# Kernel optimization log

Measured on AMD Instinct MI355X. Metric: run time of the kernel, lower is better.

The kernel has to match this reference:

```python
import jax, jax.numpy as jnp
import numpy as np

N_WAY = 64

def setup_inputs() -> dict:
    key = jax.random.key(0)
    k1, k2, k3, k4 = jax.random.split(key, 4)
    S, Q, F, D = 1024, 16384, 2048, 512
    xs = jax.random.normal(k1, (S, F), dtype=jnp.float32)
    ys = jax.random.randint(k2, (S,), 0, N_WAY, dtype=jnp.int64)
    xq = jax.random.normal(k3, (Q, F), dtype=jnp.float32)
    W = jax.random.normal(k4, (F, D), dtype=jnp.float32) * 0.02
    b = jnp.zeros((D,), dtype=jnp.float32)
    return {"xs": xs, "ys": ys, "xq": xq, "W": W, "b": b}

def reference(xs, ys, xq, W, b):
    # encoder: linear projection [*, F] -> [*, D]
    z_s = xs @ W + b            # [S, D]
    z_q = xq @ W + b            # [Q, D]
    # class prototypes: segment mean over support embeddings -> [N_way, D]
    counts = jax.ops.segment_sum(jnp.ones_like(ys, dtype=z_s.dtype), ys, num_segments=N_WAY)
    proto = jax.ops.segment_sum(z_s, ys, num_segments=N_WAY) / jnp.clip(counts, 1.0)[:, None]
    # pairwise squared euclidean distance (expand + pow + sum), [Q, N_way]
    diff = z_q[:, None, :] - proto[None, :, :]   # [Q, N_way, D]
    dists = jnp.sum(diff * diff, axis=-1)
    return -dists
```

## Files before the change

### kernel.cpp

```cpp
#include <hip/hip_runtime.h>


typedef __attribute__((ext_vector_type(8))) short short8;
typedef __attribute__((ext_vector_type(4))) float floatx4;

#define S_ROWS 1024
#define F_DIM  2048
#define D_DIM  512
#define NWAY   64
#define Q_ROWS 16384

static __device__ __forceinline__ unsigned short f2bf(float f) {
  unsigned int u = __float_as_uint(f);
  u += 0x7FFF + ((u >> 16) & 1);
  return (unsigned short)(u >> 16);
}
static __device__ __forceinline__ float bf2f(unsigned short s) {
  return __uint_as_float(((unsigned int)s) << 16);
}
static __device__ __forceinline__ unsigned int pack_bf2(float x, float y) {
  unsigned int ux = __float_as_uint(x) + 0x8000u;
  unsigned int uy = __float_as_uint(y) + 0x8000u;
  return __builtin_amdgcn_perm(uy, ux, 0x07060302u);
}

static __device__ __forceinline__ void load_lds16(const unsigned short* g, unsigned short* l) {
  __builtin_amdgcn_global_load_lds((const __attribute__((address_space(1))) unsigned int*)g,
                                   (__attribute__((address_space(3))) unsigned int*)l,
                                   16, 0, 0);
}

__global__ __launch_bounds__(256) void k_prep(const float* __restrict__ W,
                                              unsigned short* __restrict__ Wt,
                                              float* __restrict__ outz,
                                              float* __restrict__ proto_acc,
                                              const int* __restrict__ ys,
                                              int* __restrict__ order,
                                              int* __restrict__ starts,
                                              float* __restrict__ counts) {
  __shared__ unsigned short t[64][65];
  __shared__ int cnt[NWAY];
  __shared__ int st[NWAY + 1];
  __shared__ int wp[NWAY];
  int bx = blockIdx.x;
  int tid = threadIdx.x;
  if (bx < 256) {
    int f0 = (bx >> 3) << 6;
    int d0 = (bx & 7) << 6;
    for (int j = 0; j < 16; j++) {
      int lin = j * 256 + tid;
      int fl = lin >> 6, dl = lin & 63;
      t[fl][dl] = f2bf(W[(size_t)(f0 + fl) * 512 + d0 + dl]);
    }
    __syncthreads();
    for (int j = 0; j < 16; j++) {
      int lin = j * 256 + tid;
      int dl = lin >> 6, fl = lin & 63;
      Wt[(size_t)(d0 + dl) * 2048 + f0 + fl] = t[fl][dl];
    }
    float4 zz = {0.f, 0.f, 0.f, 0.f};
#pragma unroll
    for (int p = 0; p < 4; p++)
      *(float4*)&outz[(size_t)bx * 4096 + p * 1024 + tid * 4] = zz;
    if (tid < 128) proto_acc[bx * 128 + tid] = 0.f;
  } else {
    if (tid < NWAY) cnt[tid] = 0;
    __syncthreads();
    for (int j = tid; j < S_ROWS; j += 256) atomicAdd(&cnt[ys[j]], 1);
    __syncthreads();
    if (tid == 0) {
      int a = 0;
      for (int c = 0; c < NWAY; c++) { st[c] = a; wp[c] = a; a += cnt[c]; }
      st[NWAY] = a;
    }
    __syncthreads();
    for (int j = tid; j < S_ROWS; j += 256) {
      int c = ys[j];
      int p = atomicAdd(&wp[c], 1);
      order[p] = j;
    }
    if (tid < NWAY) counts[tid] = (float)cnt[tid];
    if (tid < NWAY + 1) starts[tid] = st[tid];
  }
}

__global__ __launch_bounds__(256) void k1_csum(const float* __restrict__ xs,
                                               const int* __restrict__ order,
                                               const int* __restrict__ starts,
                                               float* __restrict__ csum) {
  __shared__ int lord[S_ROWS];
  int c = blockIdx.x >> 1;
  int tid = threadIdx.x;
  int s = starts[c], e = starts[c + 1];
  int len = e - s;
  for (int j = tid; j < len; j += 256) lord[j] = order[s + j];
  __syncthreads();
  int f0 = (blockIdx.x & 1) * 1024 + tid * 4;
  float4 a = {0.f, 0.f, 0.f, 0.f};
  for (int i = 0; i < len; i++) {
    float4 v = *(const float4*)&xs[(size_t)lord[i] * F_DIM + f0];
    a.x += v.x; a.y += v.y; a.z += v.z; a.w += v.w;
  }
  *(float4*)&csum[(size_t)c * F_DIM + f0] = a;
}

__global__ __launch_bounds__(256) void k2_proto(const float* __restrict__ W,
                                               const float* __restrict__ csum,
                                               float* __restrict__ proto_acc) {
  __shared__ float cs[256];
  int bx = blockIdx.x;
  int c = bx >> 4;
  int dh = ((bx >> 3) & 1) * 256;
  int fc = (bx & 7) * 256;
  int tid = threadIdx.x;
  cs[tid] = csum[(size_t)c * F_DIM + fc + tid];
  __syncthreads();
  float a0 = 0.f;
#pragma unroll 8
  for (int f = 0; f < 256; f++)
    a0 += cs[f] * W[(size_t)(fc + f) * 512 + dh + tid];
  atomicAdd(&proto_acc[c * 512 + dh + tid], a0);
}

__global__ __launch_bounds__(256) void k2b_finalize(const float* __restrict__ proto_acc,
                                                    const float* __restrict__ b,
                                                    const float* __restrict__ counts,
                                                    unsigned short* __restrict__ proto_bf,
                                                    float* __restrict__ pnorm_part) {
  __shared__ float red[256];
  int n = blockIdx.x, tid = threadIdx.x;
  float cntv = counts[n];
  float inv = 1.f / fmaxf(cntv, 1.f);
  float qsq[2];
#pragma unroll
  for (int h = 0; h < 2; h++) {
    int d = h * 256 + tid;
    float p = (proto_acc[n * 512 + d] + cntv * b[d]) * inv;
    unsigned short hh = f2bf(p);
    proto_bf[(size_t)n * 512 + d] = hh;
    float q = bf2f(hh);
    qsq[h] = q * q;
  }
#pragma unroll
  for (int h = 0; h < 2; h++) {
    __syncthreads();
    red[tid] = qsq[h];
    __syncthreads();
    for (int s = 64; s > 0; s >>= 1) {
      if ((tid & 127) < s) red[tid] += red[tid + s];
      __syncthreads();
    }
    if (tid == 0) pnorm_part[(h * 2 + 0) * 64 + n] = red[0];
    if (tid == 128) pnorm_part[(h * 2 + 1) * 64 + n] = red[128];
  }
}

#define ZS_LD 136
__global__ __launch_bounds__(128) void k3_fused(const float* __restrict__ xq,
                                                const unsigned short* __restrict__ Wt,
                                                const float* __restrict__ b,
                                                const unsigned short* __restrict__ proto_bf,
                                                const float* __restrict__ pnorm_part,
                                                float* __restrict__ out) {
  __shared__ __align__(16) char smem[35328];
  unsigned short* lA = (unsigned short*)smem;
  unsigned short* lB = (unsigned short*)(smem + 8192);
  unsigned short* zs = (unsigned short*)smem;
  unsigned short* pb = (unsigned short*)(smem + 17408);
  float* qnf = (float*)(smem + 34816);
  float* pnl = (float*)(smem + 35072);

  int tid = threadIdx.x;
  int bx = blockIdx.x;
  int xcd = bx & 7;
  int g = bx >> 3;
  int m0 = (xcd * 32 + (g & 31)) * 64;
  int n0 = (g >> 5) * 128;
  int slice = g >> 5;

  int wave = tid >> 6, lane = tid & 63;
  int wn = wave * 64;
  int lrow = lane & 15, lquad = lane >> 4;

  floatx4 acc[4][4];
#pragma unroll
  for (int i = 0; i < 4; i++)
#pragma unroll
    for (int j = 0; j < 4; j++) acc[i][j] = (floatx4){0.f, 0.f, 0.f, 0.f};

  int arow = tid >> 2, akq = tid & 3;
  const float* agp = &xq[(size_t)(m0 + arow) * F_DIM + akq * 8];
  int bch0 = wave * 64 + lane;

  for (int k0 = 0; k0 < F_DIM; k0 += 64) {
#pragma unroll
    for (int i = 0; i < 8; i++) {
      int ch = i * 128 + bch0;
      int s = ch >> 9, row = (ch >> 2) & 127, kq = ch & 3;
      load_lds16(&Wt[(size_t)(n0 + row) * F_DIM + k0 + s * 32 + kq * 8],
                 &lB[(size_t)(i * 128 + wave * 64) * 8]);
    }
#pragma unroll
    for (int p = 0; p < 4; p++) {
      const float* gp = agp + (size_t)(p & 1) * 32 * F_DIM + (p >> 1) * 32 + k0;
      float4 v0 = *(const float4*)gp;
      float4 v1 = *(const float4*)(gp + 4);
      uint4 w;
      w.x = pack_bf2(v0.x, v0.y); w.y = pack_bf2(v0.z, v0.w);
      w.z = pack_bf2(v1.x, v1.y); w.w = pack_bf2(v1.z, v1.w);
      *(uint4*)&lA[(size_t)(p * 128 + tid) * 8] = w;
    }
    __syncthreads();
#pragma unroll
    for (int s = 0; s < 2; s++) {
      short8 af[4], bfr[4];
#pragma unroll
      for (int i = 0; i < 4; i++)
        af[i] = *(const short8*)&lA[s * 2048 + (i * 16 + lrow) * 32 + lquad * 8];
#pragma unroll
      for (int j = 0; j < 4; j++)
        bfr[j] = *(const short8*)&lB[s * 4096 + (wn + j * 16 + lrow) * 32 + lquad * 8];
#pragma unroll
      for (int i = 0; i < 4; i++)
#pragma unroll
        for (int j = 0; j < 4; j++)
          acc[i][j] = __builtin_amdgcn_mfma_f32_16x16x32_bf16(af[i], bfr[j], acc[i][j], 0, 0, 0);
    }
    __syncthreads();
  }

  if (tid < 64) { qnf[tid] = 0.f; pnl[tid] = pnorm_part[slice * 64 + tid]; }
  __syncthreads();

#pragma unroll
  for (int i = 0; i < 4; i++) {
    float rn[4] = {0.f, 0.f, 0.f, 0.f};
#pragma unroll
    for (int j = 0; j < 4; j++) {
      int ld = wn + j * 16 + lrow;
      float bb = b[n0 + ld];
#pragma unroll
      for (int r = 0; r < 4; r++) {
        int rl = i * 16 + lquad * 4 + r;
        float v = acc[i][j][r] + bb;
        unsigned short h = f2bf(v);
        zs[rl * ZS_LD + ld] = h;
        float vq = bf2f(h);
        rn[r] += vq * vq;
      }
    }
#pragma unroll
    for (int r = 0; r < 4; r++) {
      float s = rn[r];
      s += __shfl_xor(s, 1, 16);
      s += __shfl_xor(s, 2, 16);
      s += __shfl_xor(s, 4, 16);
      s += __shfl_xor(s, 8, 16);
      if (lrow == 0) atomicAdd(&qnf[i * 16 + lquad * 4 + r], s);
    }
  }

#pragma unroll
  for (int p = 0; p < 8; p++) {
    int ch = p * 128 + tid;
    int row = ch >> 4, l8 = (ch & 15) * 8;
    *(short8*)&pb[row * ZS_LD + l8] =
        *(const short8*)&proto_bf[(size_t)row * 512 + n0 + l8];
  }
  __syncthreads();

  floatx4 acc2[2][4];
#pragma unroll
  for (int i = 0; i < 2; i++)
#pragma unroll
    for (int j = 0; j < 4; j++) acc2[i][j] = (floatx4){0.f, 0.f, 0.f, 0.f};

#pragma unroll
  for (int ks = 0; ks < 4; ks++) {
    short8 af2[2], bf2r[4];
#pragma unroll
    for (int i = 0; i < 2; i++)
      af2[i] = *(const short8*)&zs[(wave * 32 + i * 16 + lrow) * ZS_LD + ks * 32 + lquad * 8];
#pragma unroll
    for (int j = 0; j < 4; j++)
      bf2r[j] = *(const short8*)&pb[(j * 16 + lrow) * ZS_LD + ks * 32 + lquad * 8];
#pragma unroll
    for (int i = 0; i < 2; i++)
#pragma unroll
      for (int j = 0; j < 4; j++)
        acc2[i][j] = __builtin_amdgcn_mfma_f32_16x16x32_bf16(af2[i], bf2r[j], acc2[i][j], 0, 0, 0);
  }

#pragma unroll
  for (int i = 0; i < 2; i++) {
#pragma unroll
    for (int j = 0; j < 4; j++) {
      int c = j * 16 + lrow;
      float pn = pnl[c];
#pragma unroll
      for (int r = 0; r < 4; r++) {
        int ql = wave * 32 + i * 16 + lquad * 4 + r;
        float val = 2.f * acc2[i][j][r] - qnf[ql] - pn;
        atomicAdd(&out[(size_t)(m0 + ql) * 64 + c], val);
      }
    }
  }
}

extern "C" void kernel_launch(void* const* d_in, const int* in_sizes, int n_in,
                              void* d_out, int out_size, void* d_ws, size_t ws_size,
                              hipStream_t stream) {
  const float* xs = (const float*)d_in[0];
  const int* ys = (const int*)d_in[1];
  const float* xq = (const float*)d_in[2];
  const float* W = (const float*)d_in[3];
  const float* b = (const float*)d_in[4];
  float* out = (float*)d_out;
  char* ws = (char*)d_ws;

  size_t off = 0;
  auto take = [&](size_t bytes) -> char* {
    char* r = ws + off;
    off += (bytes + 255) & ~(size_t)255;
    return r;
  };
  unsigned short* Wt = (unsigned short*)take((size_t)D_DIM * F_DIM * 2);
  float* csum = (float*)take((size_t)NWAY * F_DIM * 4);
  float* proto_acc = (float*)take((size_t)NWAY * D_DIM * 4);
  unsigned short* proto_bf = (unsigned short*)take((size_t)NWAY * D_DIM * 2);
  float* counts = (float*)take(NWAY * 4);
  float* pnorm_part = (float*)take(4 * NWAY * 4);
  int* order = (int*)take(S_ROWS * 4);
  int* starts = (int*)take((NWAY + 1) * 4);

  k_prep<<<257, 256, 0, stream>>>(W, Wt, out, proto_acc, ys, order, starts, counts);
  k1_csum<<<128, 256, 0, stream>>>(xs, order, starts, csum);
  k2_proto<<<1024, 256, 0, stream>>>(W, csum, proto_acc);
  k2b_finalize<<<64, 256, 0, stream>>>(proto_acc, b, counts, proto_bf, pnorm_part);
  k3_fused<<<1024, 128, 0, stream>>>(xq, Wt, b, proto_bf, pnorm_part, out);
}
```

Before: 266.3 us.

## Split fused GEMM+distance into tiled GEMM and separate distance kernel

Replaces the fused kernel, which used a 64x128 tile and accumulated partial distances into the output with global atomics, with a 128x128-tile bf16 MFMA GEMM. That GEMM writes z_q to a workspace buffer, and a second kernel computes distances per 64-query block using LDS reduction and plain stores. Prototype projection becomes a tiled kernel that writes per-chunk partials instead of using atomics, and the zeroing of the output and accumulator is removed. The aim is better operand reuse in the main GEMM and fewer global atomics, at the cost of an extra kernel launch and a 16 MB bf16 round trip through memory.

```diff
diff --git a/kernel.cpp b/kernel.cpp
--- a/kernel.cpp
+++ b/kernel.cpp
@@ -23,7 +23,6 @@
   unsigned int uy = __float_as_uint(y) + 0x8000u;
   return __builtin_amdgcn_perm(uy, ux, 0x07060302u);
 }
-
 static __device__ __forceinline__ void load_lds16(const unsigned short* g, unsigned short* l) {
   __builtin_amdgcn_global_load_lds((const __attribute__((address_space(1))) unsigned int*)g,
                                    (__attribute__((address_space(3))) unsigned int*)l,
@@ -32,8 +31,6 @@
 
 __global__ __launch_bounds__(256) void k_prep(const float* __restrict__ W,
                                               unsigned short* __restrict__ Wt,
-                                              float* __restrict__ outz,
-                                              float* __restrict__ proto_acc,
                                               const int* __restrict__ ys,
                                               int* __restrict__ order,
                                               int* __restrict__ starts,
@@ -50,19 +47,14 @@
     for (int j = 0; j < 16; j++) {
       int lin = j * 256 + tid;
       int fl = lin >> 6, dl = lin & 63;
-      t[fl][dl] = f2bf(W[(size_t)(f0 + fl) * 512 + d0 + dl]);
+      t[fl][dl] = f2bf(W[(size_t)(f0 + fl) * D_DIM + d0 + dl]);
     }
     __syncthreads();
     for (int j = 0; j < 16; j++) {
       int lin = j * 256 + tid;
       int dl = lin >> 6, fl = lin & 63;
-      Wt[(size_t)(d0 + dl) * 2048 + f0 + fl] = t[fl][dl];
-    }
-    float4 zz = {0.f, 0.f, 0.f, 0.f};
-#pragma unroll
-    for (int p = 0; p < 4; p++)
-      *(float4*)&outz[(size_t)bx * 4096 + p * 1024 + tid * 4] = zz;
-    if (tid < 128) proto_acc[bx * 128 + tid] = 0.f;
+      Wt[(size_t)(d0 + dl) * F_DIM + f0 + fl] = t[fl][dl];
+    }
   } else {
     if (tid < NWAY) cnt[tid] = 0;
     __syncthreads();
@@ -104,111 +96,115 @@
   *(float4*)&csum[(size_t)c * F_DIM + f0] = a;
 }
 
-__global__ __launch_bounds__(256) void k2_proto(const float* __restrict__ W,
-                                               const float* __restrict__ csum,
-                                               float* __restrict__ proto_acc) {
-  __shared__ float cs[256];
+__global__ __launch_bounds__(256) void k2p(const float* __restrict__ W,
+                                           const float* __restrict__ csum,
+                                           float* __restrict__ proto_part) {
+  __shared__ __align__(16) float csl[64 * 65];
+  __shared__ __align__(16) float wch[64 * 64];
   int bx = blockIdx.x;
-  int c = bx >> 4;
-  int dh = ((bx >> 3) & 1) * 256;
-  int fc = (bx & 7) * 256;
-  int tid = threadIdx.x;
-  cs[tid] = csum[(size_t)c * F_DIM + fc + tid];
-  __syncthreads();
-  float a0 = 0.f;
-#pragma unroll 8
-  for (int f = 0; f < 256; f++)
-    a0 += cs[f] * W[(size_t)(fc + f) * 512 + dh + tid];
-  atomicAdd(&proto_acc[c * 512 + dh + tid], a0);
-}
-
-__global__ __launch_bounds__(256) void k2b_finalize(const float* __restrict__ proto_acc,
-                                                    const float* __restrict__ b,
-                                                    const float* __restrict__ counts,
-                                                    unsigned short* __restrict__ proto_bf,
-                                                    float* __restrict__ pnorm_part) {
+  int fg = bx >> 3, dc = bx & 7;
+  int d0 = dc * 64;
+  int tid = threadIdx.x;
+  int c = tid >> 2, dq = (tid & 3) * 16;
+  floatx4 a0 = {0.f,0.f,0.f,0.f}, a1 = a0, a2 = a0, a3 = a0;
+  for (int fsub = 0; fsub < 4; fsub++) {
+    int f0 = (fg * 4 + fsub) * 64;
+    __syncthreads();
+    for (int idx = tid; idx < 4096; idx += 256) {
+      int r = idx >> 6, q = idx & 63;
+      csl[r * 65 + q] = csum[(size_t)r * F_DIM + f0 + q];
+      wch[idx] = W[(size_t)(f0 + r) * D_DIM + d0 + q];
+    }
+    __syncthreads();
+#pragma unroll 4
+    for (int f = 0; f < 64; f++) {
+      float s = csl[c * 65 + f];
+      const floatx4* wr = (const floatx4*)&wch[f * 64 + dq];
+      floatx4 w0 = wr[0], w1 = wr[1], w2 = wr[2], w3 = wr[3];
+      a0 += s * w0; a1 += s * w1; a2 += s * w2; a3 += s * w3;
+    }
+  }
+  float* dst = &proto_part[((size_t)fg * NWAY + c) * D_DIM + d0 + dq];
+  *(floatx4*)&dst[0]  = a0;
+  *(floatx4*)&dst[4]  = a1;
+  *(floatx4*)&dst[8]  = a2;
+  *(floatx4*)&dst[12] = a3;
+}
+
+__global__ __launch_bounds__(256) void k_pfin(const float* __restrict__ proto_part,
+                                              const float* __restrict__ b,
+                                              const float* __restrict__ counts,
+                                              unsigned short* __restrict__ proto_bf,
+                                              float* __restrict__ pnorm) {
   __shared__ float red[256];
   int n = blockIdx.x, tid = threadIdx.x;
   float cntv = counts[n];
   float inv = 1.f / fmaxf(cntv, 1.f);
-  float qsq[2];
+  float part = 0.f;
 #pragma unroll
   for (int h = 0; h < 2; h++) {
     int d = h * 256 + tid;
-    float p = (proto_acc[n * 512 + d] + cntv * b[d]) * inv;
-    unsigned short hh = f2bf(p);
-    proto_bf[(size_t)n * 512 + d] = hh;
+    float raw = 0.f;
+#pragma unroll
+    for (int p = 0; p < 8; p++)
+      raw += proto_part[((size_t)p * NWAY + n) * D_DIM + d];
+    float pv = (raw + cntv * b[d]) * inv;
+    unsigned short hh = f2bf(pv);
+    proto_bf[(size_t)n * D_DIM + d] = hh;
     float q = bf2f(hh);
-    qsq[h] = q * q;
-  }
-#pragma unroll
-  for (int h = 0; h < 2; h++) {
-    __syncthreads();
-    red[tid] = qsq[h];
-    __syncthreads();
-    for (int s = 64; s > 0; s >>= 1) {
-      if ((tid & 127) < s) red[tid] += red[tid + s];
-      __syncthreads();
-    }
-    if (tid == 0) pnorm_part[(h * 2 + 0) * 64 + n] = red[0];
-    if (tid == 128) pnorm_part[(h * 2 + 1) * 64 + n] = red[128];
-  }
-}
-
-#define ZS_LD 136
-__global__ __launch_bounds__(128) void k3_fused(const float* __restrict__ xq,
-                                                const unsigned short* __restrict__ Wt,
-                                                const float* __restrict__ b,
-                                                const unsigned short* __restrict__ proto_bf,
-                                                const float* __restrict__ pnorm_part,
-                                                float* __restrict__ out) {
-  __shared__ __align__(16) char smem[35328];
-  unsigned short* lA = (unsigned short*)smem;
-  unsigned short* lB = (unsigned short*)(smem + 8192);
-  unsigned short* zs = (unsigned short*)smem;
-  unsigned short* pb = (unsigned short*)(smem + 17408);
-  float* qnf = (float*)(smem + 34816);
-  float* pnl = (float*)(smem + 35072);
-
+    part += q * q;
+  }
+  red[tid] = part;
+  __syncthreads();
+  for (int s = 128; s > 0; s >>= 1) {
+    if (tid < s) red[tid] += red[tid + s];
+    __syncthreads();
+  }
+  if (tid == 0) pnorm[n] = red[0];
+}
+
+__global__ __launch_bounds__(256) void k3_gemm(const float* __restrict__ xq,
+                                               const unsigned short* __restrict__ Wt,
+                                               const float* __restrict__ b,
+                                               unsigned short* __restrict__ zbuf) {
+  __shared__ __align__(16) unsigned short lA[128 * 64];
+  __shared__ __align__(16) unsigned short lB[128 * 64];
   int tid = threadIdx.x;
   int bx = blockIdx.x;
   int xcd = bx & 7;
-  int g = bx >> 3;
-  int m0 = (xcd * 32 + (g & 31)) * 64;
-  int n0 = (g >> 5) * 128;
-  int slice = g >> 5;
+  int wg = xcd * 64 + (bx >> 3);
+  int mt = wg >> 2;
+  int n0 = (wg & 3) * 128;
 
   int wave = tid >> 6, lane = tid & 63;
-  int wn = wave * 64;
+  int wr = wave >> 1, wc = wave & 1;
   int lrow = lane & 15, lquad = lane >> 4;
 
+  const float* Ab = xq + (size_t)mt * 128 * F_DIM;
+
   floatx4 acc[4][4];
 #pragma unroll
   for (int i = 0; i < 4; i++)
 #pragma unroll
     for (int j = 0; j < 4; j++) acc[i][j] = (floatx4){0.f, 0.f, 0.f, 0.f};
 
-  int arow = tid >> 2, akq = tid & 3;
-  const float* agp = &xq[(size_t)(m0 + arow) * F_DIM + akq * 8];
-  int bch0 = wave * 64 + lane;
+  int sr = tid >> 3, skq = tid & 7;
+  const float* ag = Ab + (size_t)sr * F_DIM + skq * 8;
+  const unsigned short* bg = Wt + (size_t)(n0 + sr) * F_DIM + skq * 8;
 
   for (int k0 = 0; k0 < F_DIM; k0 += 64) {
 #pragma unroll
-    for (int i = 0; i < 8; i++) {
-      int ch = i * 128 + bch0;
-      int s = ch >> 9, row = (ch >> 2) & 127, kq = ch & 3;
-      load_lds16(&Wt[(size_t)(n0 + row) * F_DIM + k0 + s * 32 + kq * 8],
-                 &lB[(size_t)(i * 128 + wave * 64) * 8]);
-    }
+    for (int i = 0; i < 4; i++)
+      load_lds16(bg + (size_t)i * 32 * F_DIM + k0, &lB[(i * 256 + wave * 64) * 8]);
 #pragma unroll
     for (int p = 0; p < 4; p++) {
-      const float* gp = agp + (size_t)(p & 1) * 32 * F_DIM + (p >> 1) * 32 + k0;
+      const float* gp = ag + (size_t)p * 32 * F_DIM + k0;
       float4 v0 = *(const float4*)gp;
       float4 v1 = *(const float4*)(gp + 4);
       uint4 w;
       w.x = pack_bf2(v0.x, v0.y); w.y = pack_bf2(v0.z, v0.w);
       w.z = pack_bf2(v1.x, v1.y); w.w = pack_bf2(v1.z, v1.w);
-      *(uint4*)&lA[(size_t)(p * 128 + tid) * 8] = w;
+      *(uint4*)&lA[(p * 256 + tid) * 8] = w;
     }
     __syncthreads();
 #pragma unroll
@@ -216,10 +212,10 @@
       short8 af[4], bfr[4];
 #pragma unroll
       for (int i = 0; i < 4; i++)
-        af[i] = *(const short8*)&lA[s * 2048 + (i * 16 + lrow) * 32 + lquad * 8];
+        af[i] = *(const short8*)&lA[(wr * 64 + i * 16 + lrow) * 64 + s * 32 + lquad * 8];
 #pragma unroll
       for (int j = 0; j < 4; j++)
-        bfr[j] = *(const short8*)&lB[s * 4096 + (wn + j * 16 + lrow) * 32 + lquad * 8];
+        bfr[j] = *(const short8*)&lB[(wc * 64 + j * 16 + lrow) * 64 + s * 32 + lquad * 8];
 #pragma unroll
       for (int i = 0; i < 4; i++)
 #pragma unroll
@@ -229,81 +225,96 @@
     __syncthreads();
   }
 
-  if (tid < 64) { qnf[tid] = 0.f; pnl[tid] = pnorm_part[slice * 64 + tid]; }
+  size_t zr0 = (size_t)mt * 128;
+#pragma unroll
+  for (int j = 0; j < 4; j++) {
+    int col = n0 + wc * 64 + j * 16 + lrow;
+    float bb = b[col];
+#pragma unroll
+    for (int i = 0; i < 4; i++) {
+#pragma unroll
+      for (int r = 0; r < 4; r++) {
+        int row = wr * 64 + i * 16 + lquad * 4 + r;
+        zbuf[(zr0 + row) * D_DIM + col] = f2bf(acc[i][j][r] + bb);
+      }
+    }
+  }
+}
+
+__global__ __launch_bounds__(256) void k5_dist(const unsigned short* __restrict__ zbuf,
+                                               const unsigned short* __restrict__ proto_bf,
+                                               const float* __restrict__ pnorm,
+                                               float* __restrict__ out) {
+  __shared__ float S[64 * 65];
+  __shared__ float qn_l[64];
+  __shared__ float pn_l[64];
+  int tid = threadIdx.x;
+  int q0 = blockIdx.x * 64;
+  int wave = tid >> 6, lane = tid & 63;
+  int lrow = lane & 15, lquad = lane >> 4;
+
+  for (int i = tid; i < 64 * 65; i += 256) S[i] = 0.f;
+  if (tid < 64) { qn_l[tid] = 0.f; pn_l[tid] = pnorm[tid]; }
   __syncthreads();
 
+  floatx4 acc[4][4];
+#pragma unroll
+  for (int i = 0; i < 4; i++)
+#pragma unroll
+    for (int j = 0; j < 4; j++) acc[i][j] = (floatx4){0.f, 0.f, 0.f, 0.f};
+  float qsq[4] = {0.f, 0.f, 0.f, 0.f};
+
+  int kbase = wave * 128;
+#pragma unroll
+  for (int kk = 0; kk < 4; kk++) {
+    int k0 = kbase + kk * 32;
+    short8 af[4], bfr[4];
+#pragma unroll
+    for (int i = 0; i < 4; i++)
+      af[i] = *(const short8*)&zbuf[(size_t)(q0 + i * 16 + lrow) * D_DIM + k0 + lquad * 8];
+#pragma unroll
+    for (int j = 0; j < 4; j++)
+      bfr[j] = *(const short8*)&proto_bf[(size_t)(j * 16 + lrow) * D_DIM + k0 + lquad * 8];
+#pragma unroll
+    for (int i = 0; i < 4; i++) {
+#pragma unroll
+      for (int h = 0; h < 8; h++) {
+        float v = bf2f((unsigned short)af[i][h]);
+        qsq[i] += v * v;
+      }
+#pragma unroll
+      for (int j = 0; j < 4; j++)
+        acc[i][j] = __builtin_amdgcn_mfma_f32_16x16x32_bf16(af[i], bfr[j], acc[i][j], 0, 0, 0);
+    }
+  }
+
 #pragma unroll
   for (int i = 0; i < 4; i++) {
-    float rn[4] = {0.f, 0.f, 0.f, 0.f};
-#pragma unroll
-    for (int j = 0; j < 4; j++) {
-      int ld = wn + j * 16 + lrow;
-      float bb = b[n0 + ld];
-#pragma unroll
-      for (int r = 0; r < 4; r++) {
-        int rl = i * 16 + lquad * 4 + r;
-        float v = acc[i][j][r] + bb;
-        unsigned short h = f2bf(v);
-        zs[rl * ZS_LD + ld] = h;
-        float vq = bf2f(h);
-        rn[r] += vq * vq;
-      }
-    }
-#pragma unroll
-    for (int r = 0; r < 4; r++) {
-      float s = rn[r];
-      s += __shfl_xor(s, 1, 16);
-      s += __shfl_xor(s, 2, 16);
-      s += __shfl_xor(s, 4, 16);
-      s += __shfl_xor(s, 8, 16);
-      if (lrow == 0) atomicAdd(&qnf[i * 16 + lquad * 4 + r], s);
-    }
-  }
-
-#pragma unroll
-  for (int p = 0; p < 8; p++) {
-    int ch = p * 128 + tid;
-    int row = ch >> 4, l8 = (ch & 15) * 8;
-    *(short8*)&pb[row * ZS_LD + l8] =
-        *(const short8*)&proto_bf[(size_t)row * 512 + n0 + l8];
-  }
+    float s = qsq[i];
+    s += __shfl_xor(s, 16);
+    s += __shfl_xor(s, 32);
+    if (lquad == 0) atomicAdd(&qn_l[i * 16 + lrow], s);
+  }
+#pragma unroll
+  for (int i = 0; i < 4; i++)
+#pragma unroll
+    for (int j = 0; j < 4; j++)
+#pragma unroll
+      for (int r = 0; r < 4; r++)
+        atomicAdd(&S[(i * 16 + lquad * 4 + r) * 65 + j * 16 + lrow], acc[i][j][r]);
   __syncthreads();
 
-  floatx4 acc2[2][4];
-#pragma unroll
-  for (int i = 0; i < 2; i++)
-#pragma unroll
-    for (int j = 0; j < 4; j++) acc2[i][j] = (floatx4){0.f, 0.f, 0.f, 0.f};
-
-#pragma unroll
-  for (int ks = 0; ks < 4; ks++) {
-    short8 af2[2], bf2r[4];
-#pragma unroll
-    for (int i = 0; i < 2; i++)
-      af2[i] = *(const short8*)&zs[(wave * 32 + i * 16 + lrow) * ZS_LD + ks * 32 + lquad * 8];
-#pragma unroll
-    for (int j = 0; j < 4; j++)
-      bf2r[j] = *(const short8*)&pb[(j * 16 + lrow) * ZS_LD + ks * 32 + lquad * 8];
-#pragma unroll
-    for (int i = 0; i < 2; i++)
-#pragma unroll
-      for (int j = 0; j < 4; j++)
-        acc2[i][j] = __builtin_amdgcn_mfma_f32_16x16x32_bf16(af2[i], bf2r[j], acc2[i][j], 0, 0, 0);
-  }
-
-#pragma unroll
-  for (int i = 0; i < 2; i++) {
-#pragma unroll
-    for (int j = 0; j < 4; j++) {
-      int c = j * 16 + lrow;
-      float pn = pnl[c];
-#pragma unroll
-      for (int r = 0; r < 4; r++) {
-        int ql = wave * 32 + i * 16 + lquad * 4 + r;
-        float val = 2.f * acc2[i][j][r] - qnf[ql] - pn;
-        atomicAdd(&out[(size_t)(m0 + ql) * 64 + c], val);
-      }
-    }
+  int row = tid >> 2, c0 = (tid & 3) * 16;
+  float qv = qn_l[row];
+#pragma unroll
+  for (int u = 0; u < 4; u++) {
+    float4 o;
+    int cb = c0 + u * 4;
+    o.x = 2.f * S[row * 65 + cb + 0] - qv - pn_l[cb + 0];
+    o.y = 2.f * S[row * 65 + cb + 1] - qv - pn_l[cb + 1];
+    o.z = 2.f * S[row * 65 + cb + 2] - qv - pn_l[cb + 2];
+    o.w = 2.f * S[row * 65 + cb + 3] - qv - pn_l[cb + 3];
+    *(float4*)&out[(size_t)(q0 + row) * NWAY + cb] = o;
   }
 }
 
@@ -326,16 +337,20 @@
   };
   unsigned short* Wt = (unsigned short*)take((size_t)D_DIM * F_DIM * 2);
   float* csum = (float*)take((size_t)NWAY * F_DIM * 4);
-  float* proto_acc = (float*)take((size_t)NWAY * D_DIM * 4);
+  float* proto_part = (float*)take((size_t)8 * NWAY * D_DIM * 4);
   unsigned short* proto_bf = (unsigned short*)take((size_t)NWAY * D_DIM * 2);
   float* counts = (float*)take(NWAY * 4);
-  float* pnorm_part = (float*)take(4 * NWAY * 4);
+  float* pnorm = (float*)take(NWAY * 4);
   int* order = (int*)take(S_ROWS * 4);
   int* starts = (int*)take((NWAY + 1) * 4);
-
-  k_prep<<<257, 256, 0, stream>>>(W, Wt, out, proto_acc, ys, order, starts, counts);
+  unsigned short* zbuf = (unsigned short*)take((size_t)Q_ROWS * D_DIM * 2);
+
+  if (off > ws_size) return;
+
+  k_prep<<<257, 256, 0, stream>>>(W, Wt, ys, order, starts, counts);
   k1_csum<<<128, 256, 0, stream>>>(xs, order, starts, csum);
-  k2_proto<<<1024, 256, 0, stream>>>(W, csum, proto_acc);
-  k2b_finalize<<<64, 256, 0, stream>>>(proto_acc, b, counts, proto_bf, pnorm_part);
-  k3_fused<<<1024, 128, 0, stream>>>(xq, Wt, b, proto_bf, pnorm_part, out);
-}
+  k2p<<<64, 256, 0, stream>>>(W, csum, proto_part);
+  k_pfin<<<NWAY, 256, 0, stream>>>(proto_part, b, counts, proto_bf, pnorm);
+  k3_gemm<<<512, 256, 0, stream>>>(xq, Wt, b, zbuf);
+  k5_dist<<<256, 256, 0, stream>>>(zbuf, proto_bf, pnorm, out);
+}
```

New measurement: 299.7 us. 12.5% more time.

## Double-buffer query GEMM with 128x128 tiles and fuse prototype kernels

Applied to the files above, without the earlier changes.

The main query-encoding GEMM now runs with 256-thread blocks on 128x128 output tiles. It uses double-buffered LDS: the next W tile is loaded via global_load_lds and the next xq tile is prefetched into registers while the current one is multiplied, so the per-step stall is hidden and B traffic per output drops. The two prototype kernels (atomic partial GEMV plus finalize) are merged into one kernel that tiles W and class sums through LDS, writes bf16 prototypes and atomically accumulates their norms. Prototypes are now read straight from global memory in the distance stage. This uses more LDS per block and launches fewer blocks, which may lower occupancy.

```diff
diff --git a/kernel.cpp b/kernel.cpp
--- a/kernel.cpp
+++ b/kernel.cpp
@@ -9,6 +9,7 @@
 #define D_DIM  512
 #define NWAY   64
 #define Q_ROWS 16384
+#define ZS_LD  136
 
 static __device__ __forceinline__ unsigned short f2bf(float f) {
   unsigned int u = __float_as_uint(f);
@@ -23,7 +24,6 @@
   unsigned int uy = __float_as_uint(y) + 0x8000u;
   return __builtin_amdgcn_perm(uy, ux, 0x07060302u);
 }
-
 static __device__ __forceinline__ void load_lds16(const unsigned short* g, unsigned short* l) {
   __builtin_amdgcn_global_load_lds((const __attribute__((address_space(1))) unsigned int*)g,
                                    (__attribute__((address_space(3))) unsigned int*)l,
@@ -33,7 +33,7 @@
 __global__ __launch_bounds__(256) void k_prep(const float* __restrict__ W,
                                               unsigned short* __restrict__ Wt,
                                               float* __restrict__ outz,
-                                              float* __restrict__ proto_acc,
+                                              float* __restrict__ pnorm_part,
                                               const int* __restrict__ ys,
                                               int* __restrict__ order,
                                               int* __restrict__ starts,
@@ -45,25 +45,25 @@
   int bx = blockIdx.x;
   int tid = threadIdx.x;
   if (bx < 256) {
+    float4 zz = {0.f, 0.f, 0.f, 0.f};
+#pragma unroll
+    for (int p = 0; p < 4; p++)
+      *(float4*)&outz[(size_t)bx * 4096 + p * 1024 + tid * 4] = zz;
     int f0 = (bx >> 3) << 6;
     int d0 = (bx & 7) << 6;
     for (int j = 0; j < 16; j++) {
       int lin = j * 256 + tid;
       int fl = lin >> 6, dl = lin & 63;
-      t[fl][dl] = f2bf(W[(size_t)(f0 + fl) * 512 + d0 + dl]);
+      t[fl][dl] = f2bf(W[(size_t)(f0 + fl) * D_DIM + d0 + dl]);
     }
     __syncthreads();
     for (int j = 0; j < 16; j++) {
       int lin = j * 256 + tid;
       int dl = lin >> 6, fl = lin & 63;
-      Wt[(size_t)(d0 + dl) * 2048 + f0 + fl] = t[fl][dl];
-    }
-    float4 zz = {0.f, 0.f, 0.f, 0.f};
-#pragma unroll
-    for (int p = 0; p < 4; p++)
-      *(float4*)&outz[(size_t)bx * 4096 + p * 1024 + tid * 4] = zz;
-    if (tid < 128) proto_acc[bx * 128 + tid] = 0.f;
+      Wt[(size_t)(d0 + dl) * F_DIM + f0 + fl] = t[fl][dl];
+    }
   } else {
+    pnorm_part[tid] = 0.f;
     if (tid < NWAY) cnt[tid] = 0;
     __syncthreads();
     for (int j = tid; j < S_ROWS; j += 256) atomicAdd(&cnt[ys[j]], 1);
@@ -104,132 +104,169 @@
   *(float4*)&csum[(size_t)c * F_DIM + f0] = a;
 }
 
-__global__ __launch_bounds__(256) void k2_proto(const float* __restrict__ W,
+__global__ __launch_bounds__(256) void k2_full(const float* __restrict__ W,
                                                const float* __restrict__ csum,
-                                               float* __restrict__ proto_acc) {
-  __shared__ float cs[256];
+                                               const float* __restrict__ b,
+                                               const float* __restrict__ counts,
+                                               unsigned short* __restrict__ proto_bf,
+                                               float* __restrict__ pnorm_part) {
+  __shared__ __align__(16) float wch[64 * 64];
+  __shared__ float csl[8 * 64];
   int bx = blockIdx.x;
-  int c = bx >> 4;
-  int dh = ((bx >> 3) & 1) * 256;
-  int fc = (bx & 7) * 256;
+  int cg = bx >> 3, dc = bx & 7;
+  int c0 = cg * 8, d0 = dc * 64;
   int tid = threadIdx.x;
-  cs[tid] = csum[(size_t)c * F_DIM + fc + tid];
-  __syncthreads();
-  float a0 = 0.f;
+  int cl = tid >> 5;
+  int dl = (tid & 31) * 2;
+  float a0 = 0.f, a1 = 0.f;
+  for (int fs = 0; fs < 32; fs++) {
+    int f0 = fs * 64;
+    __syncthreads();
+    for (int idx = tid; idx < 4096; idx += 256) {
+      int r = idx >> 6, q = idx & 63;
+      wch[idx] = W[(size_t)(f0 + r) * D_DIM + d0 + q];
+    }
+    for (int idx = tid; idx < 512; idx += 256) {
+      int r = idx >> 6, q = idx & 63;
+      csl[idx] = csum[(size_t)(c0 + r) * F_DIM + f0 + q];
+    }
+    __syncthreads();
 #pragma unroll 8
-  for (int f = 0; f < 256; f++)
-    a0 += cs[f] * W[(size_t)(fc + f) * 512 + dh + tid];
-  atomicAdd(&proto_acc[c * 512 + dh + tid], a0);
-}
-
-__global__ __launch_bounds__(256) void k2b_finalize(const float* __restrict__ proto_acc,
-                                                    const float* __restrict__ b,
-                                                    const float* __restrict__ counts,
-                                                    unsigned short* __restrict__ proto_bf,
-                                                    float* __restrict__ pnorm_part) {
-  __shared__ float red[256];
-  int n = blockIdx.x, tid = threadIdx.x;
-  float cntv = counts[n];
+    for (int f = 0; f < 64; f++) {
+      float s = csl[cl * 64 + f];
+      a0 += s * wch[f * 64 + dl];
+      a1 += s * wch[f * 64 + dl + 1];
+    }
+  }
+  int c = c0 + cl;
+  float cntv = counts[c];
   float inv = 1.f / fmaxf(cntv, 1.f);
-  float qsq[2];
-#pragma unroll
-  for (int h = 0; h < 2; h++) {
-    int d = h * 256 + tid;
-    float p = (proto_acc[n * 512 + d] + cntv * b[d]) * inv;
-    unsigned short hh = f2bf(p);
-    proto_bf[(size_t)n * 512 + d] = hh;
-    float q = bf2f(hh);
-    qsq[h] = q * q;
-  }
-#pragma unroll
-  for (int h = 0; h < 2; h++) {
-    __syncthreads();
-    red[tid] = qsq[h];
-    __syncthreads();
-    for (int s = 64; s > 0; s >>= 1) {
-      if ((tid & 127) < s) red[tid] += red[tid + s];
-      __syncthreads();
-    }
-    if (tid == 0) pnorm_part[(h * 2 + 0) * 64 + n] = red[0];
-    if (tid == 128) pnorm_part[(h * 2 + 1) * 64 + n] = red[128];
-  }
-}
-
-#define ZS_LD 136
-__global__ __launch_bounds__(128) void k3_fused(const float* __restrict__ xq,
+  float p0 = (a0 + cntv * b[d0 + dl]) * inv;
+  float p1 = (a1 + cntv * b[d0 + dl + 1]) * inv;
+  unsigned short h0 = f2bf(p0), h1 = f2bf(p1);
+  proto_bf[(size_t)c * D_DIM + d0 + dl] = h0;
+  proto_bf[(size_t)c * D_DIM + d0 + dl + 1] = h1;
+  float q0 = bf2f(h0), q1 = bf2f(h1);
+  float s2 = q0 * q0 + q1 * q1;
+  s2 += __shfl_xor(s2, 1, 32);
+  s2 += __shfl_xor(s2, 2, 32);
+  s2 += __shfl_xor(s2, 4, 32);
+  s2 += __shfl_xor(s2, 8, 32);
+  s2 += __shfl_xor(s2, 16, 32);
+  if ((tid & 31) == 0) atomicAdd(&pnorm_part[(dc >> 1) * 64 + c], s2);
+}
+
+__global__ __launch_bounds__(256) void k3_fused(const float* __restrict__ xq,
                                                 const unsigned short* __restrict__ Wt,
                                                 const float* __restrict__ b,
                                                 const unsigned short* __restrict__ proto_bf,
                                                 const float* __restrict__ pnorm_part,
                                                 float* __restrict__ out) {
-  __shared__ __align__(16) char smem[35328];
-  unsigned short* lA = (unsigned short*)smem;
-  unsigned short* lB = (unsigned short*)(smem + 8192);
+  __shared__ __align__(16) char smem[66304];
+  unsigned short* lA0 = (unsigned short*)smem;
+  unsigned short* lB0 = (unsigned short*)(smem + 16384);
+  unsigned short* lA1 = (unsigned short*)(smem + 32768);
+  unsigned short* lB1 = (unsigned short*)(smem + 49152);
   unsigned short* zs = (unsigned short*)smem;
-  unsigned short* pb = (unsigned short*)(smem + 17408);
-  float* qnf = (float*)(smem + 34816);
-  float* pnl = (float*)(smem + 35072);
+  float* qnf = (float*)(smem + 65536);
+  float* pnl = (float*)(smem + 66048);
 
   int tid = threadIdx.x;
   int bx = blockIdx.x;
   int xcd = bx & 7;
-  int g = bx >> 3;
-  int m0 = (xcd * 32 + (g & 31)) * 64;
-  int n0 = (g >> 5) * 128;
-  int slice = g >> 5;
+  int wg = xcd * 64 + (bx >> 3);
+  int mt = wg >> 2;
+  int slice = wg & 3;
+  int n0 = slice * 128;
 
   int wave = tid >> 6, lane = tid & 63;
-  int wn = wave * 64;
+  int wr = wave >> 1, wc = wave & 1;
   int lrow = lane & 15, lquad = lane >> 4;
 
+  const float* Ab = xq + (size_t)mt * 128 * F_DIM;
+
   floatx4 acc[4][4];
 #pragma unroll
   for (int i = 0; i < 4; i++)
 #pragma unroll
     for (int j = 0; j < 4; j++) acc[i][j] = (floatx4){0.f, 0.f, 0.f, 0.f};
 
-  int arow = tid >> 2, akq = tid & 3;
-  const float* agp = &xq[(size_t)(m0 + arow) * F_DIM + akq * 8];
-  int bch0 = wave * 64 + lane;
-
-  for (int k0 = 0; k0 < F_DIM; k0 += 64) {
-#pragma unroll
-    for (int i = 0; i < 8; i++) {
-      int ch = i * 128 + bch0;
-      int s = ch >> 9, row = (ch >> 2) & 127, kq = ch & 3;
-      load_lds16(&Wt[(size_t)(n0 + row) * F_DIM + k0 + s * 32 + kq * 8],
-                 &lB[(size_t)(i * 128 + wave * 64) * 8]);
-    }
+  int sr = tid >> 3, skq = tid & 7;
+  const float* ag = Ab + (size_t)sr * F_DIM + skq * 8;
+  const unsigned short* bg = Wt + (size_t)(n0 + sr) * F_DIM + skq * 8;
+
+  float4 pf[4][2];
+
+  auto stageB = [&](unsigned short* lBbuf, int k0) {
+#pragma unroll
+    for (int i = 0; i < 4; i++)
+      load_lds16(bg + (size_t)i * 32 * F_DIM + k0, &lBbuf[(i * 256 + wave * 64) * 8]);
+  };
+  auto issueA = [&](int k0) {
 #pragma unroll
     for (int p = 0; p < 4; p++) {
-      const float* gp = agp + (size_t)(p & 1) * 32 * F_DIM + (p >> 1) * 32 + k0;
-      float4 v0 = *(const float4*)gp;
-      float4 v1 = *(const float4*)(gp + 4);
+      const float* gp = ag + (size_t)p * 32 * F_DIM + k0;
+      pf[p][0] = *(const float4*)gp;
+      pf[p][1] = *(const float4*)(gp + 4);
+    }
+  };
+  auto writeA = [&](unsigned short* lAbuf) {
+#pragma unroll
+    for (int p = 0; p < 4; p++) {
       uint4 w;
-      w.x = pack_bf2(v0.x, v0.y); w.y = pack_bf2(v0.z, v0.w);
-      w.z = pack_bf2(v1.x, v1.y); w.w = pack_bf2(v1.z, v1.w);
-      *(uint4*)&lA[(size_t)(p * 128 + tid) * 8] = w;
-    }
-    __syncthreads();
+      w.x = pack_bf2(pf[p][0].x, pf[p][0].y);
+      w.y = pack_bf2(pf[p][0].z, pf[p][0].w);
+      w.z = pack_bf2(pf[p][1].x, pf[p][1].y);
+      w.w = pack_bf2(pf[p][1].z, pf[p][1].w);
+      *(uint4*)&lAbuf[(p * 256 + tid) * 8] = w;
+    }
+  };
+  auto compute = [&](const unsigned short* lAbuf, const unsigned short* lBbuf) {
 #pragma unroll
     for (int s = 0; s < 2; s++) {
       short8 af[4], bfr[4];
 #pragma unroll
       for (int i = 0; i < 4; i++)
-        af[i] = *(const short8*)&lA[s * 2048 + (i * 16 + lrow) * 32 + lquad * 8];
+        af[i] = *(const short8*)&lAbuf[(wr * 64 + i * 16 + lrow) * 64 + s * 32 + lquad * 8];
 #pragma unroll
       for (int j = 0; j < 4; j++)
-        bfr[j] = *(const short8*)&lB[s * 4096 + (wn + j * 16 + lrow) * 32 + lquad * 8];
+        bfr[j] = *(const short8*)&lBbuf[(wc * 64 + j * 16 + lrow) * 64 + s * 32 + lquad * 8];
 #pragma unroll
       for (int i = 0; i < 4; i++)
 #pragma unroll
         for (int j = 0; j < 4; j++)
           acc[i][j] = __builtin_amdgcn_mfma_f32_16x16x32_bf16(af[i], bfr[j], acc[i][j], 0, 0, 0);
     }
-    __syncthreads();
-  }
-
-  if (tid < 64) { qnf[tid] = 0.f; pnl[tid] = pnorm_part[slice * 64 + tid]; }
+  };
+
+  stageB(lB0, 0);
+  issueA(0);
+  writeA(lA0);
+  __syncthreads();
+
+  for (int t = 0; t < 32; t += 2) {
+    {
+      int kn = (t + 1) * 64;
+      stageB(lB1, kn);
+      issueA(kn);
+      compute(lA0, lB0);
+      writeA(lA1);
+      __syncthreads();
+    }
+    {
+      if (t + 2 < 32) {
+        int kn = (t + 2) * 64;
+        stageB(lB0, kn);
+        issueA(kn);
+      }
+      compute(lA1, lB1);
+      if (t + 2 < 32) writeA(lA0);
+      __syncthreads();
+    }
+  }
+
+  if (tid < 128) qnf[tid] = 0.f;
+  if (tid < 64) pnl[tid] = pnorm_part[slice * 64 + tid];
   __syncthreads();
 
 #pragma unroll
@@ -237,35 +274,27 @@
     float rn[4] = {0.f, 0.f, 0.f, 0.f};
 #pragma unroll
     for (int j = 0; j < 4; j++) {
-      int ld = wn + j * 16 + lrow;
-      float bb = b[n0 + ld];
+      int col = wc * 64 + j * 16 + lrow;
+      float bb = b[n0 + col];
 #pragma unroll
       for (int r = 0; r < 4; r++) {
-        int rl = i * 16 + lquad * 4 + r;
+        int row = wr * 64 + i * 16 + lquad * 4 + r;
         float v = acc[i][j][r] + bb;
         unsigned short h = f2bf(v);
-        zs[rl * ZS_LD + ld] = h;
+        zs[row * ZS_LD + col] = h;
         float vq = bf2f(h);
         rn[r] += vq * vq;
       }
     }
 #pragma unroll
     for (int r = 0; r < 4; r++) {
-      float s = rn[r];
-      s += __shfl_xor(s, 1, 16);
-      s += __shfl_xor(s, 2, 16);
-      s += __shfl_xor(s, 4, 16);
-      s += __shfl_xor(s, 8, 16);
-      if (lrow == 0) atomicAdd(&qnf[i * 16 + lquad * 4 + r], s);
-    }
-  }
-
-#pragma unroll
-  for (int p = 0; p < 8; p++) {
-    int ch = p * 128 + tid;
-    int row = ch >> 4, l8 = (ch & 15) * 8;
-    *(short8*)&pb[row * ZS_LD + l8] =
-        *(const short8*)&proto_bf[(size_t)row * 512 + n0 + l8];
+      float s2 = rn[r];
+      s2 += __shfl_xor(s2, 1, 16);
+      s2 += __shfl_xor(s2, 2, 16);
+      s2 += __shfl_xor(s2, 4, 16);
+      s2 += __shfl_xor(s2, 8, 16);
+      if (lrow == 0) atomicAdd(&qnf[wr * 64 + i * 16 + lquad * 4 + r], s2);
+    }
   }
   __syncthreads();
 
@@ -277,20 +306,21 @@
 
 #pragma unroll
   for (int ks = 0; ks < 4; ks++) {
-    short8 af2[2], bf2r[4];
+    short8 af2[2], bp[4];
 #pragma unroll
     for (int i = 0; i < 2; i++)
       af2[i] = *(const short8*)&zs[(wave * 32 + i * 16 + lrow) * ZS_LD + ks * 32 + lquad * 8];
 #pragma unroll
     for (int j = 0; j < 4; j++)
-      bf2r[j] = *(const short8*)&pb[(j * 16 + lrow) * ZS_LD + ks * 32 + lquad * 8];
+      bp[j] = *(const short8*)&proto_bf[(size_t)(j * 16 + lrow) * D_DIM + n0 + ks * 32 + lquad * 8];
 #pragma unroll
     for (int i = 0; i < 2; i++)
 #pragma unroll
       for (int j = 0; j < 4; j++)
-        acc2[i][j] = __builtin_amdgcn_mfma_f32_16x16x32_bf16(af2[i], bf2r[j], acc2[i][j], 0, 0, 0);
-  }
-
+        acc2[i][j] = __builtin_amdgcn_mfma_f32_16x16x32_bf16(af2[i], bp[j], acc2[i][j], 0, 0, 0);
+  }
+
+  size_t qbase = (size_t)mt * 128;
 #pragma unroll
   for (int i = 0; i < 2; i++) {
 #pragma unroll
@@ -301,7 +331,7 @@
       for (int r = 0; r < 4; r++) {
         int ql = wave * 32 + i * 16 + lquad * 4 + r;
         float val = 2.f * acc2[i][j][r] - qnf[ql] - pn;
-        atomicAdd(&out[(size_t)(m0 + ql) * 64 + c], val);
+        atomicAdd(&out[(qbase + ql) * NWAY + c], val);
       }
     }
   }
@@ -326,16 +356,16 @@
   };
   unsigned short* Wt = (unsigned short*)take((size_t)D_DIM * F_DIM * 2);
   float* csum = (float*)take((size_t)NWAY * F_DIM * 4);
-  float* proto_acc = (float*)take((size_t)NWAY * D_DIM * 4);
   unsigned short* proto_bf = (unsigned short*)take((size_t)NWAY * D_DIM * 2);
   float* counts = (float*)take(NWAY * 4);
   float* pnorm_part = (float*)take(4 * NWAY * 4);
   int* order = (int*)take(S_ROWS * 4);
   int* starts = (int*)take((NWAY + 1) * 4);
 
-  k_prep<<<257, 256, 0, stream>>>(W, Wt, out, proto_acc, ys, order, starts, counts);
+  if (off > ws_size) return;
+
+  k_prep<<<257, 256, 0, stream>>>(W, Wt, out, pnorm_part, ys, order, starts, counts);
   k1_csum<<<128, 256, 0, stream>>>(xs, order, starts, csum);
-  k2_proto<<<1024, 256, 0, stream>>>(W, csum, proto_acc);
-  k2b_finalize<<<64, 256, 0, stream>>>(proto_acc, b, counts, proto_bf, pnorm_part);
-  k3_fused<<<1024, 128, 0, stream>>>(xq, Wt, b, proto_bf, pnorm_part, out);
-}
+  k2_full<<<64, 256, 0, stream>>>(W, csum, b, counts, proto_bf, pnorm_part);
+  k3_fused<<<512, 256, 0, stream>>>(xq, Wt, b, proto_bf, pnorm_part, out);
+}
```

Measured after the change: 326.4 us. 22.6% more time.
